# Performance work log

Measured on AMD Instinct MI355X. Metric: run time of the kernel, lower is better.

The kernel has to match this reference:

```python
import jax, jax.numpy as jnp
import numpy as np

B, L, D_MODEL = 4, 2048, 1024
D_STATE, D_CONV, EXPAND, HEADDIM = 128, 4, 2, 64
D_INNER = EXPAND * D_MODEL            # 2048
NHEADS = D_INNER // HEADDIM           # 32
CONV_DIM = D_INNER + 2 * D_STATE      # 2304
D_IN_PROJ = 2 * D_INNER + 2 * D_STATE + NHEADS  # 4448
EPS = 1e-5


def _silu(v):
    return v * jax.nn.sigmoid(v)


def setup_inputs() -> dict:
    key = jax.random.key(0)
    ks = jax.random.split(key, 8)
    x = jax.random.normal(ks[0], (B, L, D_MODEL), dtype=jnp.float32)
    ln_w = jnp.ones((D_MODEL,), jnp.float32)
    ln_b = jnp.zeros((D_MODEL,), jnp.float32)
    in_proj_w = jax.random.normal(ks[1], (D_IN_PROJ, D_MODEL), jnp.float32) * 0.02
    conv_w = jax.random.normal(ks[2], (CONV_DIM, D_CONV), jnp.float32) * 0.2
    conv_b = jnp.zeros((CONV_DIM,), jnp.float32)
    # inverse-softplus of dt sampled in [1e-3, 1e-1], matching mamba2 dt init
    dt_bias = jnp.log(jnp.expm1(jax.random.uniform(ks[3], (NHEADS,), minval=0.001, maxval=0.1)))
    # A sampled uniform in [1,16], stored as log (A = -exp(A_log))
    A_log = jnp.log(jax.random.uniform(ks[4], (NHEADS,), minval=1.0, maxval=16.0))
    D = jnp.ones((NHEADS,), jnp.float32)
    rms_w = jnp.ones((D_INNER,), jnp.float32)
    out_proj_w = jax.random.normal(ks[5], (D_MODEL, D_INNER), jnp.float32) * 0.02
    return {"x": x, "ln_w": ln_w, "ln_b": ln_b, "in_proj_w": in_proj_w,
            "conv_w": conv_w, "conv_b": conv_b, "dt_bias": dt_bias,
            "A_log": A_log, "D": D, "rms_w": rms_w, "out_proj_w": out_proj_w}


def reference(x, ln_w, ln_b, in_proj_w, conv_w, conv_b, dt_bias, A_log, D, rms_w, out_proj_w):
    b = x.shape[0]
    # LayerNorm
    mu = x.mean(-1, keepdims=True)
    var = ((x - mu) ** 2).mean(-1, keepdims=True)
    u = (x - mu) * jax.lax.rsqrt(var + EPS) * ln_w + ln_b
    # input projection -> z | xBC | dt
    zxbcdt = jnp.einsum('bld,ed->ble', u, in_proj_w)
    z = zxbcdt[..., :D_INNER]
    xBC = zxbcdt[..., D_INNER:D_INNER + CONV_DIM]
    dt = jax.nn.softplus(zxbcdt[..., -NHEADS:] + dt_bias)  # (b,l,h)
    # causal depthwise conv along time (kernel D_CONV) + silu
    xpad = jnp.pad(xBC, ((0, 0), (D_CONV - 1, 0), (0, 0)))
    conv = conv_b + sum(conv_w[:, k] * xpad[:, k:k + L, :] for k in range(D_CONV))
    xBC = _silu(conv)
    xh = xBC[..., :D_INNER].reshape(b, L, NHEADS, HEADDIM)       # (b,l,h,p)
    Bm = xBC[..., D_INNER:D_INNER + D_STATE]                      # (b,l,n)
    Cm = xBC[..., D_INNER + D_STATE:]                             # (b,l,n)
    A = -jnp.exp(A_log)                                           # (h,)
    dA = jnp.exp(dt * A)                                          # (b,l,h)
    dtx = dt[..., None] * xh                                      # (b,l,h,p)

    def step(h, inp):
        dA_t, dtx_t, B_t, C_t = inp
        h = dA_t[:, :, None, None] * h + dtx_t[..., None] * B_t[:, None, None, :]
        y_t = jnp.einsum('bhpn,bn->bhp', h, C_t)
        return h, y_t

    h0 = jnp.zeros((b, NHEADS, HEADDIM, D_STATE), x.dtype)
    xs = (dA.transpose(1, 0, 2), dtx.transpose(1, 0, 2, 3),
          Bm.transpose(1, 0, 2), Cm.transpose(1, 0, 2))
    _, ys = jax.lax.scan(step, h0, xs)                            # (l,b,h,p)
    y = ys.transpose(1, 0, 2, 3) + D[None, None, :, None] * xh    # skip term
    y = y.reshape(b, L, D_INNER)
    # gated RMSNorm: rmsnorm(y * silu(z)) * weight
    g = y * _silu(z)
    g = g * jax.lax.rsqrt((g * g).mean(-1, keepdims=True) + EPS) * rms_w
    out = jnp.einsum('ble,de->bld', g, out_proj_w)
    # residual; dropout is identity in eval mode
    return out + x
```

## Files before the change

kernel.cpp:

```cpp
#include <hip/hip_runtime.h>
#include <hip/hip_bf16.h>

#define DEV __device__ __forceinline__

typedef unsigned short u16;
typedef unsigned int u32;
typedef float f32x4 __attribute__((ext_vector_type(4)));
typedef short s16x8 __attribute__((ext_vector_type(8)));

static constexpr int Bb = 4, Ll = 2048, DM = 1024, DI = 2048, NH = 32;
static constexpr int CD = 2304;
static constexpr int NP = 4384;
static constexpr int NP_PAD = 4480;
static constexpr int BL = Bb * Ll;
static constexpr int NC = 32;

DEV float u2f(u16 s) { return __uint_as_float(((u32)s) << 16); }
DEV u16 f2bu(float f) {
  __hip_bfloat16 h = __float2bfloat16(f);
  u16 s; __builtin_memcpy(&s, &h, 2); return s;
}
DEV float blo(u32 u) { return __uint_as_float(u << 16); }
DEV float bhi(u32 u) { return __uint_as_float(u & 0xffff0000u); }

DEV int swz64(int r, int k)  { return r * 64  + ((((k >> 3) ^ (r & 7))) << 3) + (k & 7); }

DEV void gl_lds16(const u16* g, u16* l) {
  __builtin_amdgcn_global_load_lds(
      (const __attribute__((address_space(1))) u32*)g,
      (__attribute__((address_space(3))) u32*)l, 16, 0, 0);
}

__global__ __launch_bounds__(256) void cvt_pad(const float* __restrict__ src,
    u16* __restrict__ dst, int total, int cols, int realRows) {
  int i = blockIdx.x * 256 + threadIdx.x;
  if (i >= total) return;
  int r = i / cols;
  dst[i] = (r < realRows) ? f2bu(src[i]) : (u16)0;
}

__global__ __launch_bounds__(256) void ln_kernel(const float* __restrict__ x,
    const float* __restrict__ w, const float* __restrict__ bia, u16* __restrict__ u) {
  int row = blockIdx.x, tid = threadIdx.x;
  const float4* xr = (const float4*)(x + (size_t)row * DM);
  float4 v = xr[tid];
  float s = v.x + v.y + v.z + v.w;
  float s2 = v.x*v.x + v.y*v.y + v.z*v.z + v.w*v.w;
  #pragma unroll
  for (int o = 32; o; o >>= 1) { s += __shfl_down(s, o); s2 += __shfl_down(s2, o); }
  __shared__ float rs[4], rs2[4];
  int wv = tid >> 6, ln = tid & 63;
  if (ln == 0) { rs[wv] = s; rs2[wv] = s2; }
  __syncthreads();
  s = rs[0] + rs[1] + rs[2] + rs[3];
  s2 = rs2[0] + rs2[1] + rs2[2] + rs2[3];
  float mu = s * (1.f / DM);
  float var = s2 * (1.f / DM) - mu * mu;
  float inv = rsqrtf(var + 1e-5f);
  float4 wv4 = ((const float4*)w)[tid], bv4 = ((const float4*)bia)[tid];
  ushort4 o;
  o.x = f2bu((v.x - mu) * inv * wv4.x + bv4.x);
  o.y = f2bu((v.y - mu) * inv * wv4.y + bv4.y);
  o.z = f2bu((v.z - mu) * inv * wv4.z + bv4.z);
  o.w = f2bu((v.w - mu) * inv * wv4.w + bv4.w);
  ((ushort4*)(u + (size_t)row * DM))[tid] = o;
}

template<int MODE>
__global__ __launch_bounds__(512, 4) void gemm2p(const u16* __restrict__ A,
    const u16* __restrict__ Bw, void* __restrict__ o0, u16* __restrict__ xbc,
    u16* __restrict__ dtraw, const float* __restrict__ resid) {
  constexpr int K = (MODE == 0) ? 1024 : 2048;
  constexpr int NT = K / 32;
  __shared__ u16 SH[24576];
  int tid = threadIdx.x, wid = tid >> 6, lane = tid & 63;
  int fr = lane & 15, fq = lane >> 4;
  int nb = blockIdx.x;
  int xcd = nb & 7, i = nb >> 3;
  int m0 = (xcd * 4 + (i & 3)) * 256;
  int n0 = (i >> 2) * 128;
  int wm = (wid >> 1) * 64, wn = (wid & 1) * 64;
  int ksrcE = (((lane & 3) ^ ((lane >> 3) & 3)) << 3);
  int lr = lane >> 2;

  f32x4 acc[4][4];
  #pragma unroll
  for (int a = 0; a < 4; a++)
    #pragma unroll
    for (int b = 0; b < 4; b++) acc[a][b] = (f32x4){0.f, 0.f, 0.f, 0.f};

  auto STGA = [&](int t, int dstE) {
    #pragma unroll
    for (int h = 0; h < 2; h++) {
      int r0 = h * 128 + wid * 16;
      gl_lds16(A + (size_t)(m0 + r0 + lr) * K + t * 32 + ksrcE, &SH[dstE + r0 * 32]);
    }
  };
  auto STGB = [&](int t, int dstE) {
    int r0 = wid * 16;
    gl_lds16(Bw + (size_t)(n0 + r0 + lr) * K + t * 32 + ksrcE, &SH[dstE + r0 * 32]);
  };

  STGA(0, 0);
  STGB(0, 16384);
  asm volatile("s_waitcnt vmcnt(0)\n\ts_barrier" ::: "memory");
  for (int t = 0; t < NT; t++) {
    int ca = (t & 1) * 8192, cbf = 16384 + (t & 1) * 4096;
    if (t < NT - 1) {
      STGA(t + 1, ((t + 1) & 1) * 8192);
      STGB(t + 1, 16384 + ((t + 1) & 1) * 4096);
      asm volatile("s_waitcnt vmcnt(3)\n\ts_barrier" ::: "memory");
    } else {
      asm volatile("s_waitcnt vmcnt(0)\n\ts_barrier" ::: "memory");
    }
    s16x8 bB[4];
    #pragma unroll
    for (int nf = 0; nf < 4; nf++) {
      int rb = wn + nf * 16 + fr;
      bB[nf] = *(const s16x8*)&SH[cbf + rb * 32 + ((fq ^ ((rb >> 1) & 3)) << 3)];
    }
    __builtin_amdgcn_s_setprio(1);
    #pragma unroll
    for (int mf = 0; mf < 4; mf++) {
      int ra = wm + mf * 16 + fr;
      s16x8 af = *(const s16x8*)&SH[ca + ra * 32 + ((fq ^ ((ra >> 1) & 3)) << 3)];
      #pragma unroll
      for (int nf = 0; nf < 4; nf++)
        acc[mf][nf] = __builtin_amdgcn_mfma_f32_16x16x32_bf16(af, bB[nf], acc[mf][nf], 0, 0, 0);
    }
    __builtin_amdgcn_s_setprio(0);
    asm volatile("s_barrier" ::: "memory");
  }
  if (MODE == 0) {
    u16* zbuf = (u16*)o0;
    #pragma unroll
    for (int mf = 0; mf < 4; mf++) {
      #pragma unroll
      for (int nf = 0; nf < 4; nf++) {
        int col = n0 + wn + nf * 16 + fr;
        #pragma unroll
        for (int r = 0; r < 4; r++) {
          int row = m0 + wm + mf * 16 + fq * 4 + r;
          float v = acc[mf][nf][r];
          if (col < 2048)       zbuf[(size_t)row * 2048 + col] = f2bu(v);
          else if (col < 4352)  xbc[(size_t)row * 2304 + (col - 2048)] = f2bu(v);
          else if (col < 4384)  dtraw[(size_t)row * 32 + (col - 4352)] = f2bu(v);
        }
      }
    }
  } else {
    float* of = (float*)o0;
    #pragma unroll
    for (int mf = 0; mf < 4; mf++) {
      #pragma unroll
      for (int nf = 0; nf < 4; nf++) {
        int col = n0 + wn + nf * 16 + fr;
        #pragma unroll
        for (int r = 0; r < 4; r++) {
          int row = m0 + wm + mf * 16 + fq * 4 + r;
          of[(size_t)row * 1024 + col] = acc[mf][nf][r] + resid[(size_t)row * 1024 + col];
        }
      }
    }
  }
}

__global__ __launch_bounds__(256) void conv_silu(const u16* __restrict__ xbc,
    const float* __restrict__ cw, const float* __restrict__ cb, u16* __restrict__ out) {
  int i = blockIdx.x * 256 + threadIdx.x;
  if (i >= BL * (CD / 8)) return;
  int c8 = i % (CD / 8);
  int bl = i / (CD / 8);
  int l = bl & (Ll - 1);
  int c0 = c8 * 8;
  uint4 R[4];
  #pragma unroll
  for (int k = 0; k < 4; k++) {
    int ls = l - 3 + k;
    if (ls >= 0) R[k] = *(const uint4*)(xbc + (size_t)(bl - 3 + k) * CD + c0);
    else         R[k] = (uint4){0u, 0u, 0u, 0u};
  }
  u16 o[8];
  #pragma unroll
  for (int e = 0; e < 8; e++) {
    float acc = cb[c0 + e];
    float4 wv = *(const float4*)(cw + (size_t)(c0 + e) * 4);
    float wk[4] = {wv.x, wv.y, wv.z, wv.w};
    #pragma unroll
    for (int k = 0; k < 4; k++) {
      u32 word = (&R[k].x)[e >> 1];
      float xv = (e & 1) ? bhi(word) : blo(word);
      acc += wk[k] * xv;
    }
    float sg = 1.f / (1.f + __expf(-acc));
    o[e] = f2bu(acc * sg);
  }
  uint4 ov;
  ov.x = (u32)o[0] | ((u32)o[1] << 16);
  ov.y = (u32)o[2] | ((u32)o[3] << 16);
  ov.z = (u32)o[4] | ((u32)o[5] << 16);
  ov.w = (u32)o[6] | ((u32)o[7] << 16);
  *(uint4*)(out + (size_t)bl * CD + c0) = ov;
}

__global__ __launch_bounds__(256) void dt_cumsum(const u16* __restrict__ dtraw,
    const float* __restrict__ dtb, const float* __restrict__ alog,
    float* __restrict__ dtv, float* __restrict__ sv) {
  int wid = threadIdx.x >> 6, lane = threadIdx.x & 63;
  int g = blockIdx.x * 4 + wid;
  int b = g >> 10, h = (g >> 5) & 31, c = g & 31;
  int t = c * 64 + lane;
  float raw = u2f(dtraw[(size_t)(b * Ll + t) * 32 + h]);
  float v = raw + dtb[h];
  float dt = (v > 20.f) ? v : log1pf(__expf(v));
  float a = -dt * __expf(alog[h]);
  float s = a;
  #pragma unroll
  for (int o = 1; o < 64; o <<= 1) {
    float u = __shfl_up(s, o);
    if (lane >= o) s += u;
  }
  int idx = (b * 32 + h) * Ll + t;
  dtv[idx] = dt;
  sv[idx] = s;
}

__global__ __launch_bounds__(256) void chunk_state(const u16* __restrict__ conv,
    const float* __restrict__ dtv, const float* __restrict__ sv,
    u16* __restrict__ S) {
  __shared__ u16 xsT[64 * 64];
  __shared__ u16 BT[128 * 64];
  int gid = blockIdx.x;
  int c = gid & 31, h = (gid >> 5) & 31, b = gid >> 10;
  int bh = b * 32 + h;
  int tid = threadIdx.x, w = tid >> 6, lane = tid & 63;
  int fr = lane & 15, fq = lane >> 4;
  int j = tid & 63, pg = tid >> 6;
  int tb = c * 64;
  const float* svb = sv + (size_t)bh * Ll + tb;
  const float* dvb = dtv + (size_t)bh * Ll + tb;
  const u16* cvb = conv + (size_t)(b * Ll + tb) * CD;
  float s_last = svb[63];
  float wj = __expf(s_last - svb[j]) * dvb[j];
  const u16* rowp = cvb + (size_t)j * CD;
  #pragma unroll
  for (int rep = 0; rep < 2; rep++) {
    int p0 = rep * 32 + pg * 8;
    uint4 v = *(const uint4*)(rowp + h * 64 + p0);
    u32 va[4] = {v.x, v.y, v.z, v.w};
    #pragma unroll
    for (int e = 0; e < 4; e++) {
      xsT[swz64(p0 + 2 * e, j)]     = f2bu(blo(va[e]) * wj);
      xsT[swz64(p0 + 2 * e + 1, j)] = f2bu(bhi(va[e]) * wj);
    }
  }
  #pragma unroll
  for (int rep = 0; rep < 4; rep++) {
    int n0 = rep * 32 + pg * 8;
    uint4 v = *(const uint4*)(rowp + DI + n0);
    u32 va[4] = {v.x, v.y, v.z, v.w};
    #pragma unroll
    for (int e = 0; e < 4; e++) {
      BT[swz64(n0 + 2 * e, j)]     = (u16)(va[e] & 0xffffu);
      BT[swz64(n0 + 2 * e + 1, j)] = (u16)(va[e] >> 16);
    }
  }
  __syncthreads();
  f32x4 acc[4][2];
  #pragma unroll
  for (int mi = 0; mi < 4; mi++)
    #pragma unroll
    for (int ni = 0; ni < 2; ni++) acc[mi][ni] = (f32x4){0.f, 0.f, 0.f, 0.f};
  #pragma unroll
  for (int ks = 0; ks < 2; ks++) {
    int k8 = ks * 4 + fq;
    s16x8 bfv[2];
    #pragma unroll
    for (int ni = 0; ni < 2; ni++) {
      int rb = w * 32 + ni * 16 + fr;
      bfv[ni] = *(const s16x8*)&BT[rb * 64 + ((k8 ^ (rb & 7)) << 3)];
    }
    #pragma unroll
    for (int mi = 0; mi < 4; mi++) {
      int ra = mi * 16 + fr;
      s16x8 af = *(const s16x8*)&xsT[ra * 64 + ((k8 ^ (ra & 7)) << 3)];
      #pragma unroll
      for (int ni = 0; ni < 2; ni++)
        acc[mi][ni] = __builtin_amdgcn_mfma_f32_16x16x32_bf16(af, bfv[ni], acc[mi][ni], 0, 0, 0);
    }
  }
  u16* Sc = S + (size_t)gid * 8192;
  #pragma unroll
  for (int mi = 0; mi < 4; mi++) {
    #pragma unroll
    for (int ni = 0; ni < 2; ni++) {
      int p = mi * 16 + fq * 4;
      int n = w * 32 + ni * 16 + fr;
      #pragma unroll
      for (int r = 0; r < 4; r++)
        Sc[(size_t)(p + r) * 128 + n] = f2bu(acc[mi][ni][r]);
    }
  }
}

__global__ __launch_bounds__(256) void state_pass(u16* __restrict__ S,
    const float* __restrict__ sv) {
  int bh = blockIdx.x >> 3, q = blockIdx.x & 7;
  int o = q * 1024 + threadIdx.x * 4;
  const float* svb = sv + (size_t)bh * Ll;
  u16* base = S + (size_t)bh * NC * 8192 + o;
  float acc[4] = {0.f, 0.f, 0.f, 0.f};
  for (int c = 0; c < NC; c++) {
    uint2 sc = *(const uint2*)(base + (size_t)c * 8192);
    uint2 pre;
    pre.x = (u32)f2bu(acc[0]) | ((u32)f2bu(acc[1]) << 16);
    pre.y = (u32)f2bu(acc[2]) | ((u32)f2bu(acc[3]) << 16);
    *(uint2*)(base + (size_t)c * 8192) = pre;
    float E = __expf(svb[c * 64 + 63]);
    acc[0] = E * acc[0] + blo(sc.x);
    acc[1] = E * acc[1] + bhi(sc.x);
    acc[2] = E * acc[2] + blo(sc.y);
    acc[3] = E * acc[3] + bhi(sc.y);
  }
}

__global__ __launch_bounds__(256) void chunk_out(const u16* __restrict__ conv,
    const u16* __restrict__ hstart, const float* __restrict__ dtv,
    const float* __restrict__ sv, const float* __restrict__ Dp,
    u16* __restrict__ yb) {
  __shared__ u16 Ct[64 * 128];
  __shared__ u16 Bt[64 * 128];
  __shared__ u16 Hs[64 * 128];
  __shared__ u16 xT[64 * 64];
  __shared__ u16 Ml[64 * 64];
  __shared__ float svl[64], dtl[64], pexl[64];
  int gid = blockIdx.x;
  int c = gid & 31, h = (gid >> 5) & 31, b = gid >> 10;
  int tid = threadIdx.x, w = tid >> 6, lane = tid & 63;
  int fr = lane & 15, fq = lane >> 4;
  int tb = c * 64;
  const u16* cvb = conv + ((size_t)b * Ll + tb) * CD;
  const u16* hsrc = hstart + (((size_t)(b * 32 + h)) * NC + c) * 8192;
  #pragma unroll
  for (int qq = 0; qq < 4; qq++) {
    int q = w * 4 + qq;
    int i = q * 4 + (lane >> 4);
    int s = lane & 15;
    int kc = ((s ^ (i & 7)) << 3);
    gl_lds16(cvb + (size_t)i * CD + 2176 + kc, &Ct[q * 512]);
    gl_lds16(cvb + (size_t)i * CD + 2048 + kc, &Bt[q * 512]);
    gl_lds16(hsrc + (size_t)i * 128 + kc, &Hs[q * 512]);
  }
  {
    int j = tid & 63, pg = tid >> 6;
    const u16* rowp = cvb + (size_t)j * CD + h * 64;
    #pragma unroll
    for (int rep = 0; rep < 2; rep++) {
      int p0 = rep * 32 + pg * 8;
      uint4 v = *(const uint4*)(rowp + p0);
      u32 va[4] = {v.x, v.y, v.z, v.w};
      #pragma unroll
      for (int e = 0; e < 4; e++) {
        xT[swz64(p0 + 2 * e, j)]     = (u16)(va[e] & 0xffffu);
        xT[swz64(p0 + 2 * e + 1, j)] = (u16)(va[e] >> 16);
      }
    }
  }
  if (tid < 64) {
    float s = sv[(size_t)(b * 32 + h) * Ll + tb + tid];
    svl[tid] = s;
    pexl[tid] = __expf(s);
    dtl[tid] = dtv[(size_t)(b * 32 + h) * Ll + tb + tid];
  }
  __syncthreads();
  f32x4 g2[4];
  #pragma unroll
  for (int mi = 0; mi < 4; mi++) g2[mi] = (f32x4){0.f, 0.f, 0.f, 0.f};
  int wj = w * 16;
  #pragma unroll
  for (int ks = 0; ks < 4; ks++) {
    int k8 = ks * 4 + fq;
    int rb = wj + fr;
    s16x8 bf = *(const s16x8*)&Bt[rb * 128 + ((k8 ^ (rb & 7)) << 3)];
    #pragma unroll
    for (int mi = 0; mi < 4; mi++) {
      int ra = mi * 16 + fr;
      s16x8 af = *(const s16x8*)&Ct[ra * 128 + ((k8 ^ (ra & 7)) << 3)];
      g2[mi] = __builtin_amdgcn_mfma_f32_16x16x32_bf16(af, bf, g2[mi], 0, 0, 0);
    }
  }
  #pragma unroll
  for (int mi = 0; mi < 4; mi++) {
    int jj = wj + fr;
    #pragma unroll
    for (int r = 0; r < 4; r++) {
      int ii = mi * 16 + fq * 4 + r;
      float v = 0.f;
      if (jj <= ii) v = g2[mi][r] * __expf(svl[ii] - svl[jj]) * dtl[jj];
      Ml[swz64(ii, jj)] = f2bu(v);
    }
  }
  __syncthreads();
  f32x4 aY[4], a4[4];
  #pragma unroll
  for (int mi = 0; mi < 4; mi++) { aY[mi] = (f32x4){0.f, 0.f, 0.f, 0.f}; a4[mi] = (f32x4){0.f, 0.f, 0.f, 0.f}; }
  int wp = w * 16;
  #pragma unroll
  for (int ks = 0; ks < 2; ks++) {
    int k8 = ks * 4 + fq;
    int rb = wp + fr;
    s16x8 bf = *(const s16x8*)&xT[rb * 64 + ((k8 ^ (rb & 7)) << 3)];
    #pragma unroll
    for (int mi = 0; mi < 4; mi++) {
      int ra = mi * 16 + fr;
      s16x8 af = *(const s16x8*)&Ml[ra * 64 + ((k8 ^ (ra & 7)) << 3)];
      aY[mi] = __builtin_amdgcn_mfma_f32_16x16x32_bf16(af, bf, aY[mi], 0, 0, 0);
    }
  }
  #pragma unroll
  for (int ks = 0; ks < 4; ks++) {
    int k8 = ks * 4 + fq;
    int rb = wp + fr;
    s16x8 bf = *(const s16x8*)&Hs[rb * 128 + ((k8 ^ (rb & 7)) << 3)];
    #pragma unroll
    for (int mi = 0; mi < 4; mi++) {
      int ra = mi * 16 + fr;
      s16x8 af = *(const s16x8*)&Ct[ra * 128 + ((k8 ^ (ra & 7)) << 3)];
      a4[mi] = __builtin_amdgcn_mfma_f32_16x16x32_bf16(af, bf, a4[mi], 0, 0, 0);
    }
  }
  float Dh = Dp[h];
  u16* yrow = yb + ((size_t)b * Ll + tb) * DI + h * 64;
  #pragma unroll
  for (int mi = 0; mi < 4; mi++) {
    int p = wp + fr;
    #pragma unroll
    for (int r = 0; r < 4; r++) {
      int i = mi * 16 + fq * 4 + r;
      float xh = u2f(xT[swz64(p, i)]);
      yrow[(size_t)i * DI + p] = f2bu(aY[mi][r] + pexl[i] * a4[mi][r] + Dh * xh);
    }
  }
}

__global__ __launch_bounds__(256) void gate_rms(const u16* __restrict__ y,
    const u16* __restrict__ zbuf, const float* __restrict__ rw, u16* __restrict__ g) {
  int bl = blockIdx.x, tid = threadIdx.x;
  uint4 yv = ((const uint4*)(y + (size_t)bl * DI))[tid];
  uint4 zv = ((const uint4*)(zbuf + (size_t)bl * DI))[tid];
  u32 ya[4] = {yv.x, yv.y, yv.z, yv.w};
  u32 za[4] = {zv.x, zv.y, zv.z, zv.w};
  float gv[8];
  float ss = 0.f;
  #pragma unroll
  for (int jx = 0; jx < 4; jx++) {
    float y0 = blo(ya[jx]), y1 = bhi(ya[jx]);
    float z0 = blo(za[jx]), z1 = bhi(za[jx]);
    float s0 = z0 / (1.f + __expf(-z0));
    float s1 = z1 / (1.f + __expf(-z1));
    gv[jx * 2] = y0 * s0; gv[jx * 2 + 1] = y1 * s1;
    ss += gv[jx * 2] * gv[jx * 2] + gv[jx * 2 + 1] * gv[jx * 2 + 1];
  }
  #pragma unroll
  for (int o = 32; o; o >>= 1) ss += __shfl_down(ss, o);
  __shared__ float red[4];
  int wv = tid >> 6, ln = tid & 63;
  if (ln == 0) red[wv] = ss;
  __syncthreads();
  ss = red[0] + red[1] + red[2] + red[3];
  float scale = rsqrtf(ss * (1.f / DI) + 1e-5f);
  const float* rwp = rw + tid * 8;
  ushort4 o0, o1;
  o0.x = f2bu(gv[0] * scale * rwp[0]); o0.y = f2bu(gv[1] * scale * rwp[1]);
  o0.z = f2bu(gv[2] * scale * rwp[2]); o0.w = f2bu(gv[3] * scale * rwp[3]);
  o1.x = f2bu(gv[4] * scale * rwp[4]); o1.y = f2bu(gv[5] * scale * rwp[5]);
  o1.z = f2bu(gv[6] * scale * rwp[6]); o1.w = f2bu(gv[7] * scale * rwp[7]);
  ushort4* gp = (ushort4*)(g + (size_t)bl * DI + tid * 8);
  gp[0] = o0; gp[1] = o1;
}

extern "C" void kernel_launch(void* const* d_in, const int* in_sizes, int n_in,
                              void* d_out, int out_size, void* d_ws, size_t ws_size,
                              hipStream_t stream) {
  const float* x    = (const float*)d_in[0];
  const float* lnw  = (const float*)d_in[1];
  const float* lnb  = (const float*)d_in[2];
  const float* w1   = (const float*)d_in[3];
  const float* cw   = (const float*)d_in[4];
  const float* cb   = (const float*)d_in[5];
  const float* dtb  = (const float*)d_in[6];
  const float* alog = (const float*)d_in[7];
  const float* Dp   = (const float*)d_in[8];
  const float* rw   = (const float*)d_in[9];
  const float* w2   = (const float*)d_in[10];

  char* ws = (char*)d_ws;
  u16*   ub     = (u16*)(ws + 0);
  u16*   W1b    = (u16*)(ws + 16777216);
  u16*   conv   = (u16*)(ws + 0);
  u16*   zbuf   = (u16*)(ws + 37748736);
  u16*   xbc    = (u16*)(ws + 71303168);
  u16*   dtraw  = (u16*)(ws + 109051904);
  u16*   Sbuf   = (u16*)(ws + 71303168);
  u16*   gb     = (u16*)(ws + 71303168);
  float* dtv    = (float*)(ws + 138412032);
  float* sv     = (float*)(ws + 139460608);
  u16*   yb     = (u16*)(ws + 140509184);
  u16*   W2b    = (u16*)(ws + 174063616);
  if (ws_size < 178257920u) return;

  float* out = (float*)d_out;

  cvt_pad<<<(NP_PAD * 1024) / 256, 256, 0, stream>>>(w1, W1b, NP_PAD * 1024, 1024, NP);
  cvt_pad<<<(1024 * 2048) / 256, 256, 0, stream>>>(w2, W2b, 1024 * 2048, 2048, 1024);
  ln_kernel<<<BL, 256, 0, stream>>>(x, lnw, lnb, ub);
  gemm2p<0><<<1120, 512, 0, stream>>>(ub, W1b, zbuf, xbc, dtraw, nullptr);
  conv_silu<<<(BL * (CD / 8)) / 256, 256, 0, stream>>>(xbc, cw, cb, conv);
  dt_cumsum<<<1024, 256, 0, stream>>>(dtraw, dtb, alog, dtv, sv);
  chunk_state<<<4096, 256, 0, stream>>>(conv, dtv, sv, Sbuf);
  state_pass<<<1024, 256, 0, stream>>>(Sbuf, sv);
  chunk_out<<<4096, 256, 0, stream>>>(conv, Sbuf, dtv, sv, Dp, yb);
  gate_rms<<<BL, 256, 0, stream>>>(yb, zbuf, rw, gb);
  gemm2p<1><<<256, 512, 0, stream>>>(gb, W2b, out, nullptr, nullptr, x);
}
```

Baseline: 327.9 us.

## Use 256x256-tile pipelined GEMM kernel for the input projection

```diff
diff --git a/kernel.cpp b/kernel.cpp
--- a/kernel.cpp
+++ b/kernel.cpp
@@ -11,7 +11,7 @@
 static constexpr int Bb = 4, Ll = 2048, DM = 1024, DI = 2048, NH = 32;
 static constexpr int CD = 2304;
 static constexpr int NP = 4384;
-static constexpr int NP_PAD = 4480;
+static constexpr int NP_PAD = 4608;
 static constexpr int BL = Bb * Ll;
 static constexpr int NC = 32;
 
@@ -66,11 +66,122 @@
   ((ushort4*)(u + (size_t)row * DM))[tid] = o;
 }
 
-template<int MODE>
+__global__ __launch_bounds__(512, 2) void gemm_in8p(const u16* __restrict__ A,
+    const u16* __restrict__ Bw, u16* __restrict__ zbuf, u16* __restrict__ xbc,
+    u16* __restrict__ dtraw) {
+  __shared__ u16 SH[65536];
+  int tid = threadIdx.x, wid = tid >> 6, lane = tid & 63;
+  int fr = lane & 15, fq = lane >> 4;
+  int nb = blockIdx.x;
+  int xcd = nb & 7, ii = nb >> 3;
+  int m0 = (xcd * 4 + (ii & 3)) * 256;
+  int n0 = (ii >> 2) * 256;
+  int wm = (wid >> 2) * 128, wn = (wid & 3) * 64;
+  int srow = lane >> 3, sslot = lane & 7;
+  int ksrc = ((sslot ^ srow) << 3);
+
+  f32x4 acc[8][4];
+  #pragma unroll
+  for (int a = 0; a < 8; a++)
+    #pragma unroll
+    for (int b = 0; b < 4; b++) acc[a][b] = (f32x4){0.f, 0.f, 0.f, 0.f};
+
+  auto STAGE = [&](int op, int buf, int t, int h) {
+    const u16* gb = op ? Bw : A;
+    int org = op ? n0 : m0;
+    int base = op * 32768 + buf * 16384;
+    #pragma unroll
+    for (int q = 0; q < 2; q++) {
+      int r0 = h * 128 + q * 64 + wid * 8;
+      gl_lds16(gb + (size_t)(org + r0 + srow) * 1024 + t * 64 + ksrc,
+               &SH[base + r0 * 64]);
+    }
+  };
+  auto LDA = [&](int buf, int q, int ml, int ks) -> s16x8 {
+    int ra = wm + q * 32 + ml * 16 + fr;
+    int k8 = ks * 4 + fq;
+    return *(const s16x8*)&SH[buf * 16384 + ra * 64 + ((k8 ^ (ra & 7)) << 3)];
+  };
+  auto LDB = [&](int buf, int nf, int ks) -> s16x8 {
+    int rb = wn + nf * 16 + fr;
+    int k8 = ks * 4 + fq;
+    return *(const s16x8*)&SH[32768 + buf * 16384 + rb * 64 + ((k8 ^ (rb & 7)) << 3)];
+  };
+
+  STAGE(1, 0, 0, 0); STAGE(1, 0, 0, 1);
+  STAGE(0, 0, 0, 0); STAGE(0, 0, 0, 1);
+  STAGE(1, 1, 1, 0); STAGE(1, 1, 1, 1);
+  asm volatile("s_waitcnt vmcnt(4)\n\ts_barrier" ::: "memory");
+
+  s16x8 bB[2][4];
+  for (int it = 0; it < 8; it++) {
+    bool nl = (it < 7);
+    #pragma unroll
+    for (int p = 0; p < 8; p++) {
+      int buf = p >> 2;
+      int q = p & 3;
+      if (q == 0) {
+        #pragma unroll
+        for (int nf = 0; nf < 4; nf++)
+          #pragma unroll
+          for (int ks = 0; ks < 2; ks++) bB[ks][nf] = LDB(buf, nf, ks);
+      }
+      s16x8 af[2][2];
+      #pragma unroll
+      for (int ml = 0; ml < 2; ml++)
+        #pragma unroll
+        for (int ks = 0; ks < 2; ks++) af[ml][ks] = LDA(buf, q, ml, ks);
+      if (p == 0) STAGE(0, 1, 2 * it + 1, 0);
+      else if (p == 1) STAGE(0, 1, 2 * it + 1, 1);
+      else if (p == 2) { if (nl) STAGE(1, 0, 2 * it + 2, 0); }
+      else if (p == 3) { if (nl) STAGE(1, 0, 2 * it + 2, 1); }
+      else if (p == 4) { if (nl) STAGE(0, 0, 2 * it + 2, 0); }
+      else if (p == 5) { if (nl) STAGE(0, 0, 2 * it + 2, 1); }
+      else if (p == 6) { if (nl) STAGE(1, 1, 2 * it + 3, 0); }
+      else             { if (nl) STAGE(1, 1, 2 * it + 3, 1); }
+      asm volatile("s_barrier" ::: "memory");
+      __builtin_amdgcn_s_setprio(1);
+      #pragma unroll
+      for (int ml = 0; ml < 2; ml++)
+        #pragma unroll
+        for (int nf = 0; nf < 4; nf++)
+          #pragma unroll
+          for (int ks = 0; ks < 2; ks++)
+            acc[q * 2 + ml][nf] = __builtin_amdgcn_mfma_f32_16x16x32_bf16(
+                af[ml][ks], bB[ks][nf], acc[q * 2 + ml][nf], 0, 0, 0);
+      __builtin_amdgcn_s_setprio(0);
+      if (p == 3) {
+        if (nl) asm volatile("s_waitcnt vmcnt(4)\n\ts_barrier" ::: "memory");
+        else    asm volatile("s_waitcnt vmcnt(0)\n\ts_barrier" ::: "memory");
+      } else if (p == 7) {
+        if (nl) asm volatile("s_waitcnt vmcnt(4)\n\ts_barrier" ::: "memory");
+        else    asm volatile("s_barrier" ::: "memory");
+      } else {
+        asm volatile("s_barrier" ::: "memory");
+      }
+    }
+  }
+  #pragma unroll
+  for (int mf = 0; mf < 8; mf++) {
+    #pragma unroll
+    for (int nf = 0; nf < 4; nf++) {
+      int col = n0 + wn + nf * 16 + fr;
+      #pragma unroll
+      for (int r = 0; r < 4; r++) {
+        int row = m0 + wm + mf * 16 + fq * 4 + r;
+        float v = acc[mf][nf][r];
+        if (col < 2048)       zbuf[(size_t)row * 2048 + col] = f2bu(v);
+        else if (col < 4352)  xbc[(size_t)row * 2304 + (col - 2048)] = f2bu(v);
+        else if (col < 4384)  dtraw[(size_t)row * 32 + (col - 4352)] = f2bu(v);
+      }
+    }
+  }
+}
+
 __global__ __launch_bounds__(512, 4) void gemm2p(const u16* __restrict__ A,
-    const u16* __restrict__ Bw, void* __restrict__ o0, u16* __restrict__ xbc,
-    u16* __restrict__ dtraw, const float* __restrict__ resid) {
-  constexpr int K = (MODE == 0) ? 1024 : 2048;
+    const u16* __restrict__ Bw, float* __restrict__ of,
+    const float* __restrict__ resid) {
+  constexpr int K = 2048;
   constexpr int NT = K / 32;
   __shared__ u16 SH[24576];
   int tid = threadIdx.x, wid = tid >> 6, lane = tid & 63;
@@ -131,35 +242,15 @@
     __builtin_amdgcn_s_setprio(0);
     asm volatile("s_barrier" ::: "memory");
   }
-  if (MODE == 0) {
-    u16* zbuf = (u16*)o0;
-    #pragma unroll
-    for (int mf = 0; mf < 4; mf++) {
-      #pragma unroll
-      for (int nf = 0; nf < 4; nf++) {
-        int col = n0 + wn + nf * 16 + fr;
-        #pragma unroll
-        for (int r = 0; r < 4; r++) {
-          int row = m0 + wm + mf * 16 + fq * 4 + r;
-          float v = acc[mf][nf][r];
-          if (col < 2048)       zbuf[(size_t)row * 2048 + col] = f2bu(v);
-          else if (col < 4352)  xbc[(size_t)row * 2304 + (col - 2048)] = f2bu(v);
-          else if (col < 4384)  dtraw[(size_t)row * 32 + (col - 4352)] = f2bu(v);
-        }
-      }
-    }
-  } else {
-    float* of = (float*)o0;
-    #pragma unroll
-    for (int mf = 0; mf < 4; mf++) {
-      #pragma unroll
-      for (int nf = 0; nf < 4; nf++) {
-        int col = n0 + wn + nf * 16 + fr;
-        #pragma unroll
-        for (int r = 0; r < 4; r++) {
-          int row = m0 + wm + mf * 16 + fq * 4 + r;
-          of[(size_t)row * 1024 + col] = acc[mf][nf][r] + resid[(size_t)row * 1024 + col];
-        }
+  #pragma unroll
+  for (int mf = 0; mf < 4; mf++) {
+    #pragma unroll
+    for (int nf = 0; nf < 4; nf++) {
+      int col = n0 + wn + nf * 16 + fr;
+      #pragma unroll
+      for (int r = 0; r < 4; r++) {
+        int row = m0 + wm + mf * 16 + fq * 4 + r;
+        of[(size_t)row * 1024 + col] = acc[mf][nf][r] + resid[(size_t)row * 1024 + col];
       }
     }
   }
@@ -514,12 +605,12 @@
   cvt_pad<<<(NP_PAD * 1024) / 256, 256, 0, stream>>>(w1, W1b, NP_PAD * 1024, 1024, NP);
   cvt_pad<<<(1024 * 2048) / 256, 256, 0, stream>>>(w2, W2b, 1024 * 2048, 2048, 1024);
   ln_kernel<<<BL, 256, 0, stream>>>(x, lnw, lnb, ub);
-  gemm2p<0><<<1120, 512, 0, stream>>>(ub, W1b, zbuf, xbc, dtraw, nullptr);
+  gemm_in8p<<<576, 512, 0, stream>>>(ub, W1b, zbuf, xbc, dtraw);
   conv_silu<<<(BL * (CD / 8)) / 256, 256, 0, stream>>>(xbc, cw, cb, conv);
   dt_cumsum<<<1024, 256, 0, stream>>>(dtraw, dtb, alog, dtv, sv);
   chunk_state<<<4096, 256, 0, stream>>>(conv, dtv, sv, Sbuf);
   state_pass<<<1024, 256, 0, stream>>>(Sbuf, sv);
   chunk_out<<<4096, 256, 0, stream>>>(conv, Sbuf, dtv, sv, Dp, yb);
   gate_rms<<<BL, 256, 0, stream>>>(yb, zbuf, rw, gb);
-  gemm2p<1><<<256, 512, 0, stream>>>(gb, W2b, out, nullptr, nullptr, x);
-}
+  gemm2p<<<256, 512, 0, stream>>>(gb, W2b, out, x);
+}
```

New measurement: 339.6 us. +3.6%, slower.
